# Performance work log

Measured on AMD Instinct MI355X. Metric: run time of the kernel, lower is better.

Reference implementation:

```python
import jax, jax.numpy as jnp
import numpy as np

DIM = 2048
RANK = 8
SCALE_INIT = 0.01
N_TOKENS = 8192


def setup_inputs() -> dict:
    key = jax.random.key(0)
    kx, ku, kv = jax.random.split(key, 3)
    x = jax.random.normal(kx, (N_TOKENS, DIM), dtype=jnp.float32)
    U = jax.random.normal(ku, (DIM, RANK), dtype=jnp.float32) * SCALE_INIT
    V = jax.random.normal(kv, (DIM, RANK), dtype=jnp.float32) * SCALE_INIT
    gate = jnp.float32(-2.0)
    return {"x": x, "U": U, "V": V, "gate": gate}


def reference(x, U, V, gate):
    # omega = (U V^T - V U^T) * sigmoid(gate)  -- skew-symmetric generator
    UV = U @ V.T                               # [dim, dim]
    omega = (UV - UV.T) * jax.nn.sigmoid(gate)
    I = jnp.eye(x.shape[-1], dtype=x.dtype)
    half = omega * 0.5
    # Cayley transform: R = (I - omega/2)^{-1} (I + omega/2)
    R = jnp.linalg.solve(I - half, I + half)   # [dim, dim]
    return x @ R.T
```

## Files before the change

### kernel.cpp

```cpp
#include <hip/hip_runtime.h>
#include <cstddef>

#define DIM 2048
#define NTOK 8192
#define NEUMANN_ITERS 6


__device__ __forceinline__ unsigned pack2bf(float lo, float hi) {
  const unsigned ul = (__float_as_uint(lo) + 0x8000u) >> 16;
  const unsigned uh = (__float_as_uint(hi) + 0x8000u) & 0xffff0000u;
  return ul | uh;
}
#define B2F_LO(w) __uint_as_float((w) << 16)
#define B2F_HI(w) __uint_as_float((w) & 0xffff0000u)

__global__ __launch_bounds__(256) void rora_gram(
    const float* __restrict__ U, const float* __restrict__ V,
    float* __restrict__ prod) {
  const int e = blockIdx.x;
  const int q = e >> 6;
  const int i = (e >> 3) & 7, j = e & 7;
  const float* A = (q == 2) ? V : U;
  const float* B = (q == 0) ? U : V;
  const int t = threadIdx.x;
  float acc = 0.f;
#pragma unroll
  for (int s = 0; s < 8; ++s) {
    const int d = s * 256 + t;
    acc = fmaf(A[d * 8 + i], B[d * 8 + j], acc);
  }
#pragma unroll
  for (int m = 1; m < 64; m <<= 1) acc += __shfl_xor(acc, m, 64);
  __shared__ float wsum[4];
  if ((t & 63) == 0) wsum[t >> 6] = acc;
  __syncthreads();
  if (t == 0) prod[e] = (wsum[0] + wsum[1]) + (wsum[2] + wsum[3]);
}

__global__ __launch_bounds__(512) void rora_fused(
    const float* __restrict__ x, const float* __restrict__ U,
    const float* __restrict__ V, const float* __restrict__ gate,
    const float* __restrict__ prod, float* __restrict__ out) {
  __shared__ uint4 uvL[2][DIM];
  __shared__ float prodS[192];
  __shared__ float Gs[16][17];
  __shared__ float Bm[16][17];
  __shared__ float Ya[16][17];
  __shared__ float Yb[16][17];
  const int t = threadIdx.x;

  {
    const float4* U4 = (const float4*)U;
    const float4* V4 = (const float4*)V;
#pragma unroll
    for (int rep = 0; rep < 4; ++rep) {
      const int d = rep * 512 + t;
      const float4 a = U4[2 * d], b = U4[2 * d + 1];
      uvL[0][d] = make_uint4(pack2bf(a.x, a.y), pack2bf(a.z, a.w),
                             pack2bf(b.x, b.y), pack2bf(b.z, b.w));
      const float4 c = V4[2 * d], e = V4[2 * d + 1];
      uvL[1][d] = make_uint4(pack2bf(c.x, c.y), pack2bf(c.z, c.w),
                             pack2bf(e.x, e.y), pack2bf(e.z, e.w));
    }
  }

  if (t < 192) prodS[t] = prod[t];
  __syncthreads();
  const float sg = 1.f / (1.f + expf(-gate[0]));
  if (t < 256) {
    const int r = t >> 4, c = t & 15;
    float g;
    if (r < 8) g = (c < 8) ? sg * prodS[64 + c * 8 + r]
                           : sg * prodS[128 + r * 8 + (c - 8)];
    else       g = (c < 8) ? -sg * prodS[(r - 8) * 8 + c]
                           : -sg * prodS[64 + (r - 8) * 8 + (c - 8)];
    const float b = ((r == c) ? 1.f : 0.f) + 0.5f * g;
    Gs[r][c] = g;
    Bm[r][c] = b;
    Ya[r][c] = b;
  }
  __syncthreads();
#pragma unroll
  for (int m = 0; m < NEUMANN_ITERS; ++m) {
    if (t < 256) {
      const int r = t >> 4, c = t & 15;
      const float (*Yp)[17] = (m & 1) ? Yb : Ya;
      float (*Yn)[17] = (m & 1) ? Ya : Yb;
      float acc = Bm[r][c];
#pragma unroll
      for (int j = 0; j < 16; ++j)
        acc = fmaf(0.5f * Gs[r][j], Yp[j][c], acc);
      Yn[r][c] = acc;
    }
    __syncthreads();
  }

  const int wv = t >> 6, lane = t & 63;
  const int row0 = blockIdx.x * 16 + wv * 2;
  const float* xr0 = x + (size_t)row0 * DIM;
  const float* xr1 = xr0 + DIM;

  float a0[16], a1[16];
#pragma unroll
  for (int k = 0; k < 16; ++k) { a0[k] = 0.f; a1[k] = 0.f; }

#pragma unroll 4
  for (int i = 0; i < 32; ++i) {
    const int d = i * 64 + lane;
    const float x0 = xr0[d], x1 = xr1[d];
    const uint4 pu = uvL[0][d], pv = uvL[1][d];
    const float uu[16] = {
        B2F_LO(pu.x), B2F_HI(pu.x), B2F_LO(pu.y), B2F_HI(pu.y),
        B2F_LO(pu.z), B2F_HI(pu.z), B2F_LO(pu.w), B2F_HI(pu.w),
        B2F_LO(pv.x), B2F_HI(pv.x), B2F_LO(pv.y), B2F_HI(pv.y),
        B2F_LO(pv.z), B2F_HI(pv.z), B2F_LO(pv.w), B2F_HI(pv.w)};
#pragma unroll
    for (int k = 0; k < 16; ++k) {
      a0[k] = fmaf(x0, uu[k], a0[k]);
      a1[k] = fmaf(x1, uu[k], a1[k]);
    }
  }

#pragma unroll
  for (int m = 1; m < 64; m <<= 1)
#pragma unroll
    for (int k = 0; k < 16; ++k) {
      a0[k] += __shfl_xor(a0[k], m, 64);
      a1[k] += __shfl_xor(a1[k], m, 64);
    }

  {
    const int kk = lane & 15;
    float zrow[16];
#pragma unroll
    for (int j = 0; j < 16; ++j)
      zrow[j] = Ya[kk][j] + ((j == kk) ? 1.f : 0.f);
    const float hs = 0.5f * sg;
    float s0 = 0.f, s1 = 0.f;
#pragma unroll
    for (int j = 0; j < 8; ++j) {
      s0 = fmaf(zrow[j], a0[8 + j], s0);
      s0 = fmaf(-zrow[8 + j], a0[j], s0);
      s1 = fmaf(zrow[j], a1[8 + j], s1);
      s1 = fmaf(-zrow[8 + j], a1[j], s1);
    }
    const float cp0 = hs * s0, cp1 = hs * s1;
#pragma unroll
    for (int k = 0; k < 16; ++k) {
      a0[k] = __shfl(cp0, k, 64);
      a1[k] = __shfl(cp1, k, 64);
    }
  }

  float* o0 = out + (size_t)row0 * DIM;
  float* o1 = o0 + DIM;
#pragma unroll 4
  for (int i = 0; i < 32; ++i) {
    const int d = i * 64 + lane;
    const float x0 = xr0[d], x1 = xr1[d];
    const uint4 pu = uvL[0][d], pv = uvL[1][d];
    const float uu[16] = {
        B2F_LO(pu.x), B2F_HI(pu.x), B2F_LO(pu.y), B2F_HI(pu.y),
        B2F_LO(pu.z), B2F_HI(pu.z), B2F_LO(pu.w), B2F_HI(pu.w),
        B2F_LO(pv.x), B2F_HI(pv.x), B2F_LO(pv.y), B2F_HI(pv.y),
        B2F_LO(pv.z), B2F_HI(pv.z), B2F_LO(pv.w), B2F_HI(pv.w)};
    float acc0 = x0, acc1 = x1;
#pragma unroll
    for (int k = 0; k < 16; ++k) {
      acc0 = fmaf(a0[k], uu[k], acc0);
      acc1 = fmaf(a1[k], uu[k], acc1);
    }
    o0[d] = acc0;
    o1[d] = acc1;
  }
}

extern "C" void kernel_launch(void* const* d_in, const int* in_sizes, int n_in,
                              void* d_out, int out_size, void* d_ws, size_t ws_size,
                              hipStream_t stream) {
  const float* x    = (const float*)d_in[0];
  const float* U    = (const float*)d_in[1];
  const float* V    = (const float*)d_in[2];
  const float* gate = (const float*)d_in[3];
  float* out = (float*)d_out;
  float* prodw = (float*)d_ws;

  rora_gram<<<192, 256, 0, stream>>>(U, V, prodw);
  rora_fused<<<NTOK / 16, 512, 0, stream>>>(x, U, V, gate, prodw, out);
}
```

Before: 48.58 us.

## Switch U/V to fp16 pairs with fdot2 projection, packed hfma2 expansion, DPP reductions

Stores U and V in shared memory as fp16 packed pairs covering adjacent dims, so each lane handles two dims per iteration with float2 loads of x. The projection uses fdot2 (fp16 dot with fp32 accumulate), the output correction uses packed half2 FMAs, and the cross-lane reductions use DPP row ops instead of full shuffles. The goal is to cut ALU and LDS instruction count in a kernel that is mostly memory-bound. In exchange, x is quantized to fp16 and the correction term is accumulated in fp16, which lowers accuracy.

Result: faster. 45.55 us (-6.2%).

```diff
diff --git a/kernel.cpp b/kernel.cpp
--- a/kernel.cpp
+++ b/kernel.cpp
@@ -1,4 +1,5 @@
 #include <hip/hip_runtime.h>
+#include <hip/hip_fp16.h>
 #include <cstddef>
 
 #define DIM 2048
@@ -6,13 +7,32 @@
 #define NEUMANN_ITERS 6
 
 
-__device__ __forceinline__ unsigned pack2bf(float lo, float hi) {
-  const unsigned ul = (__float_as_uint(lo) + 0x8000u) >> 16;
-  const unsigned uh = (__float_as_uint(hi) + 0x8000u) & 0xffff0000u;
-  return ul | uh;
-}
-#define B2F_LO(w) __uint_as_float((w) << 16)
-#define B2F_HI(w) __uint_as_float((w) & 0xffff0000u)
+typedef _Float16 h2 __attribute__((ext_vector_type(2)));
+
+__device__ __forceinline__ unsigned pkh(float lo, float hi) {
+  auto p = __builtin_amdgcn_cvt_pkrtz(lo, hi);
+  return __builtin_bit_cast(unsigned, p);
+}
+__device__ __forceinline__ h2 cvt2h(float lo, float hi) {
+  auto p = __builtin_amdgcn_cvt_pkrtz(lo, hi);
+  return __builtin_bit_cast(h2, p);
+}
+
+template <int CTRL>
+__device__ __forceinline__ float dpp_add(float v) {
+  const int t =
+      __builtin_amdgcn_update_dpp(0, __float_as_int(v), CTRL, 0xf, 0xf, true);
+  return v + __int_as_float(t);
+}
+__device__ __forceinline__ float wave_red(float v) {
+  v = dpp_add<0xB1>(v);
+  v = dpp_add<0x4E>(v);
+  v = dpp_add<0x141>(v);
+  v = dpp_add<0x140>(v);
+  v += __shfl_xor(v, 16, 64);
+  v += __shfl_xor(v, 32, 64);
+  return v;
+}
 
 __global__ __launch_bounds__(256) void rora_gram(
     const float* __restrict__ U, const float* __restrict__ V,
@@ -41,7 +61,7 @@
     const float* __restrict__ x, const float* __restrict__ U,
     const float* __restrict__ V, const float* __restrict__ gate,
     const float* __restrict__ prod, float* __restrict__ out) {
-  __shared__ uint4 uvL[2][DIM];
+  __shared__ uint4 uvQ[4][DIM / 2];
   __shared__ float prodS[192];
   __shared__ float Gs[16][17];
   __shared__ float Bm[16][17];
@@ -53,14 +73,20 @@
     const float4* U4 = (const float4*)U;
     const float4* V4 = (const float4*)V;
 #pragma unroll
-    for (int rep = 0; rep < 4; ++rep) {
-      const int d = rep * 512 + t;
-      const float4 a = U4[2 * d], b = U4[2 * d + 1];
-      uvL[0][d] = make_uint4(pack2bf(a.x, a.y), pack2bf(a.z, a.w),
-                             pack2bf(b.x, b.y), pack2bf(b.z, b.w));
-      const float4 c = V4[2 * d], e = V4[2 * d + 1];
-      uvL[1][d] = make_uint4(pack2bf(c.x, c.y), pack2bf(c.z, c.w),
-                             pack2bf(e.x, e.y), pack2bf(e.z, e.w));
+    for (int rep = 0; rep < 2; ++rep) {
+      const int P = rep * 512 + t;
+      const float4 a0 = U4[4 * P + 0], a1 = U4[4 * P + 1];
+      const float4 a2 = U4[4 * P + 2], a3 = U4[4 * P + 3];
+      const float4 b0 = V4[4 * P + 0], b1 = V4[4 * P + 1];
+      const float4 b2 = V4[4 * P + 2], b3 = V4[4 * P + 3];
+      uvQ[0][P] = make_uint4(pkh(a0.x, a2.x), pkh(a0.y, a2.y),
+                             pkh(a0.z, a2.z), pkh(a0.w, a2.w));
+      uvQ[1][P] = make_uint4(pkh(a1.x, a3.x), pkh(a1.y, a3.y),
+                             pkh(a1.z, a3.z), pkh(a1.w, a3.w));
+      uvQ[2][P] = make_uint4(pkh(b0.x, b2.x), pkh(b0.y, b2.y),
+                             pkh(b0.z, b2.z), pkh(b0.w, b2.w));
+      uvQ[3][P] = make_uint4(pkh(b1.x, b3.x), pkh(b1.y, b3.y),
+                             pkh(b1.z, b3.z), pkh(b1.w, b3.w));
     }
   }
 
@@ -97,38 +123,66 @@
 
   const int wv = t >> 6, lane = t & 63;
   const int row0 = blockIdx.x * 16 + wv * 2;
-  const float* xr0 = x + (size_t)row0 * DIM;
-  const float* xr1 = xr0 + DIM;
+  const float2* x2A = (const float2*)(x + (size_t)row0 * DIM);
+  const float2* x2B = x2A + DIM / 2;
 
   float a0[16], a1[16];
 #pragma unroll
   for (int k = 0; k < 16; ++k) { a0[k] = 0.f; a1[k] = 0.f; }
 
 #pragma unroll 4
-  for (int i = 0; i < 32; ++i) {
-    const int d = i * 64 + lane;
-    const float x0 = xr0[d], x1 = xr1[d];
-    const uint4 pu = uvL[0][d], pv = uvL[1][d];
-    const float uu[16] = {
-        B2F_LO(pu.x), B2F_HI(pu.x), B2F_LO(pu.y), B2F_HI(pu.y),
-        B2F_LO(pu.z), B2F_HI(pu.z), B2F_LO(pu.w), B2F_HI(pu.w),
-        B2F_LO(pv.x), B2F_HI(pv.x), B2F_LO(pv.y), B2F_HI(pv.y),
-        B2F_LO(pv.z), B2F_HI(pv.z), B2F_LO(pv.w), B2F_HI(pv.w)};
+  for (int i = 0; i < 16; ++i) {
+    const int P = i * 64 + lane;
+    const float2 xA = x2A[P], xB = x2B[P];
+    const uint4 qa = uvQ[0][P], qb = uvQ[1][P];
+    const uint4 qc = uvQ[2][P], qd = uvQ[3][P];
+#if __has_builtin(__builtin_amdgcn_fdot2)
+    const h2 xpA = cvt2h(xA.x, xA.y);
+    const h2 xpB = cvt2h(xB.x, xB.y);
+#define D2(acc, xp, u) \
+  acc = __builtin_amdgcn_fdot2(xp, __builtin_bit_cast(h2, u), acc, false)
+    D2(a0[0], xpA, qa.x);  D2(a0[1], xpA, qa.y);
+    D2(a0[2], xpA, qa.z);  D2(a0[3], xpA, qa.w);
+    D2(a0[4], xpA, qb.x);  D2(a0[5], xpA, qb.y);
+    D2(a0[6], xpA, qb.z);  D2(a0[7], xpA, qb.w);
+    D2(a0[8], xpA, qc.x);  D2(a0[9], xpA, qc.y);
+    D2(a0[10], xpA, qc.z); D2(a0[11], xpA, qc.w);
+    D2(a0[12], xpA, qd.x); D2(a0[13], xpA, qd.y);
+    D2(a0[14], xpA, qd.z); D2(a0[15], xpA, qd.w);
+    D2(a1[0], xpB, qa.x);  D2(a1[1], xpB, qa.y);
+    D2(a1[2], xpB, qa.z);  D2(a1[3], xpB, qa.w);
+    D2(a1[4], xpB, qb.x);  D2(a1[5], xpB, qb.y);
+    D2(a1[6], xpB, qb.z);  D2(a1[7], xpB, qb.w);
+    D2(a1[8], xpB, qc.x);  D2(a1[9], xpB, qc.y);
+    D2(a1[10], xpB, qc.z); D2(a1[11], xpB, qc.w);
+    D2(a1[12], xpB, qd.x); D2(a1[13], xpB, qd.y);
+    D2(a1[14], xpB, qd.z); D2(a1[15], xpB, qd.w);
+#undef D2
+#else
+    const __half2 uu[16] = {
+        __builtin_bit_cast(__half2, qa.x), __builtin_bit_cast(__half2, qa.y),
+        __builtin_bit_cast(__half2, qa.z), __builtin_bit_cast(__half2, qa.w),
+        __builtin_bit_cast(__half2, qb.x), __builtin_bit_cast(__half2, qb.y),
+        __builtin_bit_cast(__half2, qb.z), __builtin_bit_cast(__half2, qb.w),
+        __builtin_bit_cast(__half2, qc.x), __builtin_bit_cast(__half2, qc.y),
+        __builtin_bit_cast(__half2, qc.z), __builtin_bit_cast(__half2, qc.w),
+        __builtin_bit_cast(__half2, qd.x), __builtin_bit_cast(__half2, qd.y),
+        __builtin_bit_cast(__half2, qd.z), __builtin_bit_cast(__half2, qd.w)};
 #pragma unroll
     for (int k = 0; k < 16; ++k) {
-      a0[k] = fmaf(x0, uu[k], a0[k]);
-      a1[k] = fmaf(x1, uu[k], a1[k]);
-    }
-  }
-
-#pragma unroll
-  for (int m = 1; m < 64; m <<= 1)
-#pragma unroll
-    for (int k = 0; k < 16; ++k) {
-      a0[k] += __shfl_xor(a0[k], m, 64);
-      a1[k] += __shfl_xor(a1[k], m, 64);
-    }
-
+      a0[k] = fmaf(xA.x, __low2float(uu[k]), fmaf(xA.y, __high2float(uu[k]), a0[k]));
+      a1[k] = fmaf(xB.x, __low2float(uu[k]), fmaf(xB.y, __high2float(uu[k]), a1[k]));
+    }
+#endif
+  }
+
+#pragma unroll
+  for (int k = 0; k < 16; ++k) {
+    a0[k] = wave_red(a0[k]);
+    a1[k] = wave_red(a1[k]);
+  }
+
+  __half2 ch0[16], ch1[16];
   {
     const int kk = lane & 15;
     float zrow[16];
@@ -147,31 +201,36 @@
     const float cp0 = hs * s0, cp1 = hs * s1;
 #pragma unroll
     for (int k = 0; k < 16; ++k) {
-      a0[k] = __shfl(cp0, k, 64);
-      a1[k] = __shfl(cp1, k, 64);
-    }
-  }
-
-  float* o0 = out + (size_t)row0 * DIM;
-  float* o1 = o0 + DIM;
+      ch0[k] = __float2half2_rn(__shfl(cp0, k, 64));
+      ch1[k] = __float2half2_rn(__shfl(cp1, k, 64));
+    }
+  }
+
+  float2* o2A = (float2*)(out + (size_t)row0 * DIM);
+  float2* o2B = o2A + DIM / 2;
+  const __half2 hz = __float2half2_rn(0.f);
 #pragma unroll 4
-  for (int i = 0; i < 32; ++i) {
-    const int d = i * 64 + lane;
-    const float x0 = xr0[d], x1 = xr1[d];
-    const uint4 pu = uvL[0][d], pv = uvL[1][d];
-    const float uu[16] = {
-        B2F_LO(pu.x), B2F_HI(pu.x), B2F_LO(pu.y), B2F_HI(pu.y),
-        B2F_LO(pu.z), B2F_HI(pu.z), B2F_LO(pu.w), B2F_HI(pu.w),
-        B2F_LO(pv.x), B2F_HI(pv.x), B2F_LO(pv.y), B2F_HI(pv.y),
-        B2F_LO(pv.z), B2F_HI(pv.z), B2F_LO(pv.w), B2F_HI(pv.w)};
-    float acc0 = x0, acc1 = x1;
-#pragma unroll
-    for (int k = 0; k < 16; ++k) {
-      acc0 = fmaf(a0[k], uu[k], acc0);
-      acc1 = fmaf(a1[k], uu[k], acc1);
-    }
-    o0[d] = acc0;
-    o1[d] = acc1;
+  for (int i = 0; i < 16; ++i) {
+    const int P = i * 64 + lane;
+    const uint4 qa = uvQ[0][P], qb = uvQ[1][P];
+    const uint4 qc = uvQ[2][P], qd = uvQ[3][P];
+    __half2 sA = hz, sB = hz;
+#define HF(u, k)                                               \
+  sA = __hfma2(ch0[k], __builtin_bit_cast(__half2, u), sA);    \
+  sB = __hfma2(ch1[k], __builtin_bit_cast(__half2, u), sB)
+    HF(qa.x, 0);  HF(qa.y, 1);  HF(qa.z, 2);  HF(qa.w, 3);
+    HF(qb.x, 4);  HF(qb.y, 5);  HF(qb.z, 6);  HF(qb.w, 7);
+    HF(qc.x, 8);  HF(qc.y, 9);  HF(qc.z, 10); HF(qc.w, 11);
+    HF(qd.x, 12); HF(qd.y, 13); HF(qd.z, 14); HF(qd.w, 15);
+#undef HF
+    const float2 xA = x2A[P], xB = x2B[P];
+    float2 oA, oB;
+    oA.x = xA.x + __low2float(sA);
+    oA.y = xA.y + __high2float(sA);
+    oB.x = xB.x + __low2float(sB);
+    oB.y = xB.y + __high2float(sB);
+    o2A[P] = oA;
+    o2B[P] = oB;
   }
 }
 
```
